# Performance work log

Measured on AMD Instinct MI355X. Metric: run time of the kernel, lower is better.

## Reference

```python
import jax, jax.numpy as jnp
import numpy as np

B, S, HID = 2, 2048, 4096
NH, NKV = 32, 8
HD = HID // NH          # 128
G = NH // NKV           # 4 groups per kv head
ROPE_THETA = 10000.0


def setup_inputs() -> dict:
    key = jax.random.key(0)
    ks = jax.random.split(key, 5)
    scale = 0.02
    return {
        "hidden_states": jax.random.normal(ks[0], (B, S, HID), dtype=jnp.float32),
        "Wq": jax.random.normal(ks[1], (NH * HD, HID), dtype=jnp.float32) * scale,
        "Wk": jax.random.normal(ks[2], (NKV * HD, HID), dtype=jnp.float32) * scale,
        "Wv": jax.random.normal(ks[3], (NKV * HD, HID), dtype=jnp.float32) * scale,
        "Wo": jax.random.normal(ks[4], (HID, HID), dtype=jnp.float32) * scale,
    }


def _rope_cos_sin(seq_len, head_dim, dtype):
    inv_freq = 1.0 / (ROPE_THETA ** (jnp.arange(0, head_dim, 2, dtype=jnp.float32) / head_dim))
    pos = jnp.arange(seq_len, dtype=jnp.float32)
    freqs = pos[:, None] * inv_freq[None, :]          # [S, HD/2]
    emb = jnp.concatenate([freqs, freqs], axis=-1)    # [S, HD]  (Llama: duplicated halves)
    return jnp.cos(emb).astype(dtype), jnp.sin(emb).astype(dtype)


def _rotate_half(x):
    x1, x2 = jnp.split(x, 2, axis=-1)
    return jnp.concatenate([-x2, x1], axis=-1)


def _apply_rope(x, cos, sin):
    # x: [B, H, S, HD]; cos/sin: [S, HD]
    return x * cos[None, None] + _rotate_half(x) * sin[None, None]


def reference(hidden_states, Wq, Wk, Wv, Wo):
    bsz, q_len, _ = hidden_states.shape
    dt = hidden_states.dtype

    q = (hidden_states @ Wq.T).reshape(bsz, q_len, NH, HD).transpose(0, 2, 1, 3)    # [B,NH,S,HD]
    k = (hidden_states @ Wk.T).reshape(bsz, q_len, NKV, HD).transpose(0, 2, 1, 3)   # [B,NKV,S,HD]
    v = (hidden_states @ Wv.T).reshape(bsz, q_len, NKV, HD).transpose(0, 2, 1, 3)   # [B,NKV,S,HD]

    cos, sin = _rope_cos_sin(q_len, HD, dt)
    q = _apply_rope(q, cos, sin)
    k = _apply_rope(k, cos, sin)

    # GQA: group queries per kv head instead of materializing repeat_kv
    qg = q.reshape(bsz, NKV, G, q_len, HD)                                          # [B,NKV,G,S,HD]
    scores = jnp.einsum("bkgqd,bkvd->bkgqv", qg, k) * (1.0 / np.sqrt(HD))           # [B,NKV,G,S,S]

    causal = jnp.tril(jnp.ones((q_len, q_len), dtype=bool))
    scores = jnp.where(causal[None, None, None], scores, jnp.finfo(jnp.float32).min)

    probs = jax.nn.softmax(scores.astype(jnp.float32), axis=-1).astype(dt)
    out = jnp.einsum("bkgqv,bkvd->bkgqd", probs, v)                                 # [B,NKV,G,S,HD]
    out = out.reshape(bsz, NH, q_len, HD).transpose(0, 2, 1, 3).reshape(bsz, q_len, HID)
    return out @ Wo.T
```

## Files before the change

### kernel.cpp

```cpp
#include <hip/hip_runtime.h>

typedef unsigned short u16;
typedef unsigned int u32;
typedef __attribute__((ext_vector_type(8))) short short8;
typedef __attribute__((ext_vector_type(4))) float f32x4;
typedef __attribute__((ext_vector_type(4))) u16 ushort4_t;

__device__ __forceinline__ float bf2f(u16 u) {
    u32 x = ((u32)u) << 16;
    return __uint_as_float(x);
}
__device__ __forceinline__ u16 f2bf(float f) {
    u32 x = __float_as_uint(f);
    x += 0x7FFFu + ((x >> 16) & 1u);
    return (u16)(x >> 16);
}
__device__ __forceinline__ u32 cvtpk_bf16(float lo, float hi) {
    u32 r;
    asm("v_cvt_pk_bf16_f32 %0, %1, %2" : "=v"(r) : "v"(lo), "v"(hi));
    return r;
}
__device__ __forceinline__ float exp2_hw(float x) {
    float r;
    asm("v_exp_f32 %0, %1" : "=v"(r) : "v"(x));
    return r;
}

using as1_cv = __attribute__((address_space(1))) const void;
using as3_v  = __attribute__((address_space(3))) void;
__device__ __forceinline__ void gld16(const void* g, void* l) {
    __builtin_amdgcn_global_load_lds((as1_cv*)g, (as3_v*)l, 16, 0, 0);
}

__global__ void cvt_f32_bf16(const float* __restrict__ in, u16* __restrict__ out, int n4) {
    int i = blockIdx.x * 256 + threadIdx.x;
    if (i >= n4) return;
    float4 v = ((const float4*)in)[i];
    ushort4_t o;
    o[0] = f2bf(v.x); o[1] = f2bf(v.y); o[2] = f2bf(v.z); o[3] = f2bf(v.w);
    ((ushort4_t*)out)[i] = o;
}

template <int OUT_MODE>
__global__ __launch_bounds__(256) void gemm_bt(
    const u16* __restrict__ A, const u16* __restrict__ B,
    u16* __restrict__ Cb, float* __restrict__ Cf,
    int M, int N, int K)
{
    __shared__ __align__(16) u16 As[128 * 32];
    __shared__ __align__(16) u16 Bs[128 * 32];
    const int t    = threadIdx.x;
    const int lane = t & 63;
    const int w    = t >> 6;
    const int wm   = w & 1;
    const int wn   = w >> 1;
    const int bx   = blockIdx.x;
    const int by   = blockIdx.y;

    const int r  = t >> 2;
    const int c8 = (t & 3) * 8;
    const u16* gA0 = A + (size_t)(by * 128 + r) * K + c8;
    const u16* gA1 = gA0 + (size_t)64 * K;
    const u16* gB0 = B + (size_t)(bx * 128 + r) * K + c8;
    const u16* gB1 = gB0 + (size_t)64 * K;
    u16* lA0 = &As[t * 8];
    u16* lA1 = &As[2048 + t * 8];
    u16* lB0 = &Bs[t * 8];
    u16* lB1 = &Bs[2048 + t * 8];

    f32x4 acc[4][4] = {};

    const int arow = wm * 64 + (lane & 15);
    const int brow = wn * 64 + (lane & 15);
    const int koff = (lane >> 4) * 8;

    for (int kt = 0; kt < K; kt += 32) {
        gld16(gA0 + kt, lA0);
        gld16(gA1 + kt, lA1);
        gld16(gB0 + kt, lB0);
        gld16(gB1 + kt, lB1);
        __syncthreads();
        short8 af[4], bf[4];
#pragma unroll
        for (int i = 0; i < 4; i++)
            af[i] = *(const short8*)&As[(arow + i * 16) * 32 + koff];
#pragma unroll
        for (int i = 0; i < 4; i++)
            bf[i] = *(const short8*)&Bs[(brow + i * 16) * 32 + koff];
#pragma unroll
        for (int mi = 0; mi < 4; mi++)
#pragma unroll
            for (int ni = 0; ni < 4; ni++)
                acc[mi][ni] = __builtin_amdgcn_mfma_f32_16x16x32_bf16(
                    af[mi], bf[ni], acc[mi][ni], 0, 0, 0);
        __syncthreads();
    }

    const int row0 = by * 128 + wm * 64 + (lane >> 4) * 4;
    const int col0 = bx * 128 + wn * 64 + (lane & 15);
#pragma unroll
    for (int mi = 0; mi < 4; mi++) {
#pragma unroll
        for (int ni = 0; ni < 4; ni++) {
            if (OUT_MODE == 3) {
                ushort4_t o;
#pragma unroll
                for (int rr = 0; rr < 4; rr++) o[rr] = f2bf(acc[mi][ni][rr]);
                int col = col0 + ni * 16;
                *(ushort4_t*)&Cb[(size_t)col * M + row0 + mi * 16] = o;
            } else {
#pragma unroll
                for (int rr = 0; rr < 4; rr++) {
                    int row = row0 + mi * 16 + rr;
                    int col = col0 + ni * 16;
                    float v = acc[mi][ni][rr];
                    if (OUT_MODE == 1) Cf[(size_t)row * N + col] = v;
                    else               Cb[(size_t)row * N + col] = f2bf(v);
                }
            }
        }
    }
}

template <int OUT_MODE>
__global__ __launch_bounds__(512, 2) void gemm_bt256(
    const u16* __restrict__ A, const u16* __restrict__ B,
    u16* __restrict__ Cb, float* __restrict__ Cf,
    int M, int N, int K)
{
    __shared__ __align__(16) u16 S[65536];
    const int t    = threadIdx.x;
    const int lane = t & 63;
    const int w    = t >> 6;
    const int wm   = w >> 2;
    const int wn   = w & 3;
    const int col  = lane & 15;
    const int g    = lane >> 4;

    const int kel = (((t & 3) ^ ((t >> 4) & 3)) * 8);
    const u16* gA = A + (size_t)(blockIdx.y * 256 + (t >> 2)) * K + kel;
    const u16* gB = B + (size_t)(blockIdx.x * 256 + (t >> 2)) * K + kel;
    const size_t rstride = (size_t)128 * K;
    u16* ldsA = &S[t * 8];
    u16* ldsB = &S[8192 + t * 8];

    const int rchunk = (((col * 4 + g) ^ ((col >> 2) & 3)) * 8);
    int aoff[8], boff[4];
#pragma unroll
    for (int mi = 0; mi < 8; mi++) aoff[mi] = (wm * 8 + mi) * 512 + rchunk;
#pragma unroll
    for (int ni = 0; ni < 4; ni++) boff[ni] = 8192 + (wn * 4 + ni) * 512 + rchunk;

    f32x4 acc[8][4] = {};

    auto STAGE = [&](int slot, int kt) {
        const size_t so = (size_t)slot * 16384;
        gld16(gA + kt,            ldsA + so);
        gld16(gA + kt + rstride,  ldsA + so + 4096);
        gld16(gB + kt,            ldsB + so);
        gld16(gB + kt + rstride,  ldsB + so + 4096);
    };

    const int NT = K >> 5;
    STAGE(0, 0);
    STAGE(1, 32);
    STAGE(2, 64);

    for (int kt = 0; kt < NT; kt++) {
        if (kt < NT - 2)      asm volatile("s_waitcnt vmcnt(8)" ::: "memory");
        else if (kt < NT - 1) asm volatile("s_waitcnt vmcnt(4)" ::: "memory");
        else                  asm volatile("s_waitcnt vmcnt(0)" ::: "memory");
        __builtin_amdgcn_s_barrier();
        asm volatile("" ::: "memory");
        if (kt < NT - 3) STAGE((kt + 3) & 3, (kt + 3) << 5);

        const u16* Sb = &S[(kt & 3) * 16384];
        short8 af[8], bf[4];
#pragma unroll
        for (int mi = 0; mi < 8; mi++) af[mi] = *(const short8*)(Sb + aoff[mi]);
#pragma unroll
        for (int ni = 0; ni < 4; ni++) bf[ni] = *(const short8*)(Sb + boff[ni]);

        __builtin_amdgcn_s_setprio(1);
#pragma unroll
        for (int mi = 0; mi < 8; mi++)
#pragma unroll
            for (int ni = 0; ni < 4; ni++)
                acc[mi][ni] = __builtin_amdgcn_mfma_f32_16x16x32_bf16(
                    af[mi], bf[ni], acc[mi][ni], 0, 0, 0);
        __builtin_amdgcn_s_setprio(0);
    }

    const int row0 = blockIdx.y * 256 + wm * 128 + (lane >> 4) * 4;
    const int col0 = blockIdx.x * 256 + wn * 64 + (lane & 15);
#pragma unroll
    for (int mi = 0; mi < 8; mi++) {
#pragma unroll
        for (int ni = 0; ni < 4; ni++) {
#pragma unroll
            for (int rr = 0; rr < 4; rr++) {
                int row = row0 + mi * 16 + rr;
                int col = col0 + ni * 16;
                float v = acc[mi][ni][rr];
                if (OUT_MODE == 1) Cf[(size_t)row * N + col] = v;
                else               Cb[(size_t)row * N + col] = f2bf(v);
            }
        }
    }
}

__global__ void rope_k(u16* __restrict__ x, int hshift, float scale) {
    int idx = blockIdx.x * 256 + threadIdx.x;
    int i   = idx & 63;
    int hm  = (1 << (hshift - 6)) - 1;
    int h   = (idx >> 6) & hm;
    int row = idx >> hshift;
    int s   = row & 2047;
    int stride = (hm + 1) * 128;
    size_t base = (size_t)row * stride + h * 128 + i;
    float th = (float)s * exp2f(-(float)i * 0.20762050593045952f);
    float cs = cosf(th), sn = sinf(th);
    float x1 = bf2f(x[base]), x2 = bf2f(x[base + 64]);
    x[base]      = f2bf((x1 * cs - x2 * sn) * scale);
    x[base + 64] = f2bf((x2 * cs + x1 * sn) * scale);
}

__global__ __launch_bounds__(512) void flash_attn(
    const u16* __restrict__ qb, const u16* __restrict__ kb,
    const u16* __restrict__ vt, u16* __restrict__ ob)
{
    __shared__ __align__(16) u16 Ks[3][64 * 128];
    __shared__ __align__(16) u16 Vs[3][128 * 64];
    const int t    = threadIdx.x;
    const int lane = t & 63;
    const int w    = t >> 6;
    const int col  = lane & 15;
    const int g    = lane >> 4;
    const int p    = blockIdx.x;
    const int qh   = blockIdx.y;
    const int b    = blockIdx.z;
    const int kvh  = qh >> 2;

    const u16* kbase = kb + ((size_t)b * 2048) * 1024 + kvh * 128;
    const u16* vbase = vt + ((size_t)kvh * 128) * 4096 + (size_t)b * 2048;

    const int ksw = ((t >> 4) & 3) ^ (((t >> 4) & 8) >> 1);
    const u16* ksrc0 = kbase + (size_t)(t >> 4) * 1024 + (size_t)((t & 15) ^ ksw) * 8;
    const u16* vsrc0 = vbase + (size_t)(t >> 3) * 4096 + (size_t)(((t & 7) ^ ((t >> 3) & 7)) * 8);
    u16* kdst = &Ks[0][0] + t * 8;
    u16* vdst = &Vs[0][0] + t * 8;

    const int swr = (col & 3) ^ (((col >> 2) & 1) << 2);
    int kb_[2][2];
#pragma unroll
    for (int h = 0; h < 2; h++)
#pragma unroll
        for (int kk = 0; kk < 2; kk++)
            kb_[h][kk] = (h * 32 + (col >> 2) * 8 + kk * 4 + (col & 3)) * 16;
    int cco[4];
#pragma unroll
    for (int c = 0; c < 4; c++) cco[c] = (c * 4 + g) ^ swr;
    const int vrow = col * 8;
    const int vcc0 = (g) ^ (col & 7);
    const int vcc1 = (4 + g) ^ (col & 7);

    auto STAGE = [&](int slot, int k0i) {
        const size_t so = (size_t)slot * 8192;
        gld16(ksrc0 + (size_t)k0i * 1024,        kdst + so);
        gld16(ksrc0 + (size_t)(k0i + 32) * 1024, kdst + so + 4096);
        gld16(vsrc0 + k0i,                       vdst + so);
        gld16(vsrc0 + (size_t)64 * 4096 + k0i,   vdst + so + 4096);
    };

#pragma unroll 1
    for (int phase = 0; phase < 2; phase++) {
        const int qt = phase ? (3 - p) : (4 + p);
        const int Q0 = qt * 256;
        const int qw = Q0 + w * 32;

        short8 qf[2][4];
#pragma unroll
        for (int sub = 0; sub < 2; sub++) {
            const u16* qrow = qb + ((size_t)(b * 2048 + qw + sub * 16 + col)) * 4096 + qh * 128;
#pragma unroll
            for (int c = 0; c < 4; c++)
                qf[sub][c] = *(const short8*)(qrow + c * 32 + g * 8);
        }

        float m_run[2] = {0.f, 0.f};
        float l_run[2] = {0.f, 0.f};
        f32x4 ot[2][8] = {};

        const int nsteps = (Q0 + 256) >> 6;
        const int qmax_w = qw + 31;

        STAGE(0, 0);
        STAGE(1, 64);
        int slc = 0;

        for (int step = 0; step < nsteps; step++) {
            const int k0 = step << 6;
            if (step + 1 < nsteps) asm volatile("s_waitcnt vmcnt(4)" ::: "memory");
            else                   asm volatile("s_waitcnt vmcnt(0)" ::: "memory");
            __builtin_amdgcn_s_barrier();
            asm volatile("" ::: "memory");
            if (step + 2 < nsteps) {
                int sl2 = slc + 2; if (sl2 >= 3) sl2 -= 3;
                STAGE(sl2, (step + 2) << 6);
            }

            if (k0 <= qmax_w) {
                const u16* Kp = &Ks[slc][0];
                const u16* Vp = &Vs[slc][0];

                f32x4 sc[2][2][2] = {};
                __builtin_amdgcn_s_setprio(1);
#pragma unroll
                for (int h = 0; h < 2; h++)
#pragma unroll
                    for (int c = 0; c < 4; c++)
#pragma unroll
                        for (int kk = 0; kk < 2; kk++) {
                            short8 kf = *(const short8*)(Kp + (size_t)(kb_[h][kk] + cco[c]) * 8);
                            sc[0][h][kk] = __builtin_amdgcn_mfma_f32_16x16x32_bf16(kf, qf[0][c], sc[0][h][kk], 0, 0, 0);
                            sc[1][h][kk] = __builtin_amdgcn_mfma_f32_16x16x32_bf16(kf, qf[1][c], sc[1][h][kk], 0, 0, 0);
                        }
                __builtin_amdgcn_s_setprio(0);

                const bool full = (k0 + 63 <= qw);
                short8 pf[2][2];
#pragma unroll
                for (int sub = 0; sub < 2; sub++) {
                    float s[16];
                    float tmax = -1e30f;
                    if (full) {
#pragma unroll
                        for (int h = 0; h < 2; h++)
#pragma unroll
                            for (int kk = 0; kk < 2; kk++)
#pragma unroll
                                for (int rr = 0; rr < 4; rr++) {
                                    float v = sc[sub][h][kk][rr];
                                    s[h * 8 + kk * 4 + rr] = v;
                                    tmax = fmaxf(tmax, v);
                                }
                    } else {
                        const int q = qw + sub * 16 + col;
#pragma unroll
                        for (int h = 0; h < 2; h++)
#pragma unroll
                            for (int kk = 0; kk < 2; kk++)
#pragma unroll
                                for (int rr = 0; rr < 4; rr++) {
                                    int key = k0 + h * 32 + g * 8 + kk * 4 + rr;
                                    float v = sc[sub][h][kk][rr];
                                    v = (key <= q) ? v : -1e30f;
                                    s[h * 8 + kk * 4 + rr] = v;
                                    tmax = fmaxf(tmax, v);
                                }
                    }
                    tmax = fmaxf(tmax, __shfl_xor(tmax, 16));
                    tmax = fmaxf(tmax, __shfl_xor(tmax, 32));
                    if (__any(tmax > m_run[sub] + 8.0f)) {
                        float m_new = fmaxf(m_run[sub], tmax);
                        float alpha = exp2_hw(m_run[sub] - m_new);
                        l_run[sub] *= alpha;
                        m_run[sub] = m_new;
#pragma unroll
                        for (int dt = 0; dt < 8; dt++)
#pragma unroll
                            for (int rr = 0; rr < 4; rr++) ot[sub][dt][rr] *= alpha;
                    }
                    const float m = m_run[sub];
                    float tsum = 0.f;
#pragma unroll
                    for (int j = 0; j < 16; j++) {
                        s[j] = exp2_hw(s[j] - m);
                        tsum += s[j];
                    }
#pragma unroll
                    for (int h = 0; h < 2; h++)
#pragma unroll
                        for (int jw = 0; jw < 4; jw++)
                            ((u32*)&pf[sub][h])[jw] = cvtpk_bf16(s[h * 8 + jw * 2], s[h * 8 + jw * 2 + 1]);
                    tsum += __shfl_xor(tsum, 16);
                    tsum += __shfl_xor(tsum, 32);
                    l_run[sub] += tsum;
                }

                __builtin_amdgcn_s_setprio(1);
#pragma unroll
                for (int dt = 0; dt < 8; dt++) {
                    short8 vf0 = *(const short8*)(Vp + (size_t)(dt * 128 + vrow + vcc0) * 8);
                    short8 vf1 = *(const short8*)(Vp + (size_t)(dt * 128 + vrow + vcc1) * 8);
                    ot[0][dt] = __builtin_amdgcn_mfma_f32_16x16x32_bf16(vf0, pf[0][0], ot[0][dt], 0, 0, 0);
                    ot[1][dt] = __builtin_amdgcn_mfma_f32_16x16x32_bf16(vf0, pf[1][0], ot[1][dt], 0, 0, 0);
                    ot[0][dt] = __builtin_amdgcn_mfma_f32_16x16x32_bf16(vf1, pf[0][1], ot[0][dt], 0, 0, 0);
                    ot[1][dt] = __builtin_amdgcn_mfma_f32_16x16x32_bf16(vf1, pf[1][1], ot[1][dt], 0, 0, 0);
                }
                __builtin_amdgcn_s_setprio(0);
            }
            slc = (slc == 2) ? 0 : slc + 1;
        }
        __syncthreads();

#pragma unroll
        for (int sub = 0; sub < 2; sub++) {
            float inv = 1.0f / l_run[sub];
            u16* orow = ob + ((size_t)(b * 2048 + qw + sub * 16 + col)) * 4096 + qh * 128;
#pragma unroll
            for (int dt = 0; dt < 8; dt++) {
                ushort4_t o;
#pragma unroll
                for (int rr = 0; rr < 4; rr++) o[rr] = f2bf(ot[sub][dt][rr] * inv);
                *(ushort4_t*)(orow + dt * 16 + g * 4) = o;
            }
        }
    }
}

extern "C" void kernel_launch(void* const* d_in, const int* in_sizes, int n_in,
                              void* d_out, int out_size, void* d_ws, size_t ws_size,
                              hipStream_t stream) {
    const float* hs = (const float*)d_in[0];
    const float* Wq = (const float*)d_in[1];
    const float* Wk = (const float*)d_in[2];
    const float* Wv = (const float*)d_in[3];
    const float* Wo = (const float*)d_in[4];
    float* out = (float*)d_out;

    char* ws = (char*)d_ws;
    u16* hsb = (u16*)(ws + 0);
    u16* Wqb = (u16*)(ws + 33554432);
    u16* Wkb = (u16*)(ws + 67108864);
    u16* Wvb = (u16*)(ws + 75497472);
    u16* Wob = (u16*)(ws + 83886080);
    u16* qb  = (u16*)(ws + 117440512);
    u16* kbf = (u16*)(ws + 150994944);
    u16* vtb = (u16*)(ws + 159383552);
    u16* ab  = hsb;

    cvt_f32_bf16<<<16384, 256, 0, stream>>>(hs, hsb, 4194304);
    cvt_f32_bf16<<<16384, 256, 0, stream>>>(Wq, Wqb, 4194304);
    cvt_f32_bf16<<<4096,  256, 0, stream>>>(Wk, Wkb, 1048576);
    cvt_f32_bf16<<<4096,  256, 0, stream>>>(Wv, Wvb, 1048576);
    cvt_f32_bf16<<<16384, 256, 0, stream>>>(Wo, Wob, 4194304);

    gemm_bt256<0><<<dim3(16, 16), 512, 0, stream>>>(hsb, Wqb, qb,  nullptr, 4096, 4096, 4096);
    gemm_bt<0><<<dim3(8, 32),  256, 0, stream>>>(hsb, Wkb, kbf, nullptr, 4096, 1024, 4096);
    gemm_bt<3><<<dim3(8, 32),  256, 0, stream>>>(hsb, Wvb, vtb, nullptr, 4096, 1024, 4096);

    rope_k<<<32768, 256, 0, stream>>>(qb,  11, 0.08838834764831845f * 1.4426950408889634f);
    rope_k<<<8192,  256, 0, stream>>>(kbf, 9, 1.0f);

    flash_attn<<<dim3(4, 32, 2), 512, 0, stream>>>(qb, kbf, vtb, ab);

    gemm_bt256<1><<<dim3(16, 16), 512, 0, stream>>>(ab, Wob, nullptr, out, 4096, 4096, 4096);
}
```

Measured before the change: 782.4 us.

## Restructure GEMM main loop into 8-phase ping-pong schedule with interleaved loads

The 256x256 GEMM K-loop moves from a 4-slot ring of 32-wide K tiles to two 64-wide K buffers. Each iteration is split into four phases, and each phase interleaves LDS fragment reads, one half-tile global prefetch, barriers and a block of MFMAs. The aim is finer overlap of global loads, LDS reads and matrix math, with reads pinned in place by sched_barrier and setprio. The cost is many more block barriers per iteration and fragile hand-tuned vmcnt accounting that must match the issue order.

Result: no change. 796.0 us (+1.7%).

```diff
diff --git a/kernel.cpp b/kernel.cpp
--- a/kernel.cpp
+++ b/kernel.cpp
@@ -141,54 +141,107 @@
     const u16* gA = A + (size_t)(blockIdx.y * 256 + (t >> 2)) * K + kel;
     const u16* gB = B + (size_t)(blockIdx.x * 256 + (t >> 2)) * K + kel;
     const size_t rstride = (size_t)128 * K;
-    u16* ldsA = &S[t * 8];
-    u16* ldsB = &S[8192 + t * 8];
 
     const int rchunk = (((col * 4 + g) ^ ((col >> 2) & 3)) * 8);
     int aoff[8], boff[4];
 #pragma unroll
     for (int mi = 0; mi < 8; mi++) aoff[mi] = (wm * 8 + mi) * 512 + rchunk;
 #pragma unroll
-    for (int ni = 0; ni < 4; ni++) boff[ni] = 8192 + (wn * 4 + ni) * 512 + rchunk;
+    for (int ni = 0; ni < 4; ni++) boff[ni] = (wn * 4 + ni) * 512 + rchunk;
 
     f32x4 acc[8][4] = {};
 
-    auto STAGE = [&](int slot, int kt) {
-        const size_t so = (size_t)slot * 16384;
-        gld16(gA + kt,            ldsA + so);
-        gld16(gA + kt + rstride,  ldsA + so + 4096);
-        gld16(gB + kt,            ldsB + so);
-        gld16(gB + kt + rstride,  ldsB + so + 4096);
+    auto STAGE_H = [&](int b, int op, int kh, int kt) {
+        const u16* gsrc = op ? gB : gA;
+        u16* dst = &S[b * 32768 + kh * 16384 + op * 8192 + t * 8];
+        const int ko = (kt << 6) + (kh << 5);
+        gld16(gsrc + ko, dst);
+        gld16(gsrc + ko + rstride, dst + 4096);
     };
 
-    const int NT = K >> 5;
-    STAGE(0, 0);
-    STAGE(1, 32);
-    STAGE(2, 64);
+    const int NT = K >> 6;
+
+    STAGE_H(0, 0, 0, 0); STAGE_H(0, 1, 0, 0); STAGE_H(0, 0, 1, 0); STAGE_H(0, 1, 1, 0);
+    STAGE_H(1, 0, 0, 1); STAGE_H(1, 1, 0, 1); STAGE_H(1, 0, 1, 1);
+    asm volatile("s_waitcnt vmcnt(6)" ::: "memory");
+    __builtin_amdgcn_s_barrier();
 
     for (int kt = 0; kt < NT; kt++) {
-        if (kt < NT - 2)      asm volatile("s_waitcnt vmcnt(8)" ::: "memory");
-        else if (kt < NT - 1) asm volatile("s_waitcnt vmcnt(4)" ::: "memory");
-        else                  asm volatile("s_waitcnt vmcnt(0)" ::: "memory");
-        __builtin_amdgcn_s_barrier();
-        asm volatile("" ::: "memory");
-        if (kt < NT - 3) STAGE((kt + 3) & 3, (kt + 3) << 5);
-
-        const u16* Sb = &S[(kt & 3) * 16384];
-        short8 af[8], bf[4];
-#pragma unroll
-        for (int mi = 0; mi < 8; mi++) af[mi] = *(const short8*)(Sb + aoff[mi]);
-#pragma unroll
-        for (int ni = 0; ni < 4; ni++) bf[ni] = *(const short8*)(Sb + boff[ni]);
-
+        const int b = kt & 1;
+        const u16* Ak0 = &S[b * 32768];
+        const u16* Bk0 = &S[b * 32768 + 8192];
+        const u16* Ak1 = &S[b * 32768 + 16384];
+        const u16* Bk1 = &S[b * 32768 + 24576];
+
+        short8 af0[8], bf00, bf01;
+#pragma unroll
+        for (int mi = 0; mi < 8; mi++) af0[mi] = *(const short8*)(Ak0 + aoff[mi]);
+        bf00 = *(const short8*)(Bk0 + boff[0]);
+        bf01 = *(const short8*)(Bk0 + boff[1]);
+        if (kt + 1 < NT) STAGE_H(b ^ 1, 1, 1, kt + 1);
+        __builtin_amdgcn_s_barrier();
+        asm volatile("s_waitcnt lgkmcnt(0)" ::: "memory");
+        __builtin_amdgcn_sched_barrier(0);
         __builtin_amdgcn_s_setprio(1);
 #pragma unroll
-        for (int mi = 0; mi < 8; mi++)
-#pragma unroll
-            for (int ni = 0; ni < 4; ni++)
-                acc[mi][ni] = __builtin_amdgcn_mfma_f32_16x16x32_bf16(
-                    af[mi], bf[ni], acc[mi][ni], 0, 0, 0);
+        for (int mi = 0; mi < 8; mi++) {
+            acc[mi][0] = __builtin_amdgcn_mfma_f32_16x16x32_bf16(af0[mi], bf00, acc[mi][0], 0, 0, 0);
+            acc[mi][1] = __builtin_amdgcn_mfma_f32_16x16x32_bf16(af0[mi], bf01, acc[mi][1], 0, 0, 0);
+        }
         __builtin_amdgcn_s_setprio(0);
+        __builtin_amdgcn_s_barrier();
+
+        short8 bf02, bf03;
+        bf02 = *(const short8*)(Bk0 + boff[2]);
+        bf03 = *(const short8*)(Bk0 + boff[3]);
+        if (kt + 2 < NT) STAGE_H(b, 0, 0, kt + 2);
+        __builtin_amdgcn_s_barrier();
+        asm volatile("s_waitcnt lgkmcnt(0)" ::: "memory");
+        __builtin_amdgcn_sched_barrier(0);
+        __builtin_amdgcn_s_setprio(1);
+#pragma unroll
+        for (int mi = 0; mi < 8; mi++) {
+            acc[mi][2] = __builtin_amdgcn_mfma_f32_16x16x32_bf16(af0[mi], bf02, acc[mi][2], 0, 0, 0);
+            acc[mi][3] = __builtin_amdgcn_mfma_f32_16x16x32_bf16(af0[mi], bf03, acc[mi][3], 0, 0, 0);
+        }
+        __builtin_amdgcn_s_setprio(0);
+        __builtin_amdgcn_s_barrier();
+
+        short8 af1[8], bf10, bf11;
+#pragma unroll
+        for (int mi = 0; mi < 8; mi++) af1[mi] = *(const short8*)(Ak1 + aoff[mi]);
+        bf10 = *(const short8*)(Bk1 + boff[0]);
+        bf11 = *(const short8*)(Bk1 + boff[1]);
+        if (kt + 2 < NT) STAGE_H(b, 1, 0, kt + 2);
+        __builtin_amdgcn_s_barrier();
+        asm volatile("s_waitcnt lgkmcnt(0)" ::: "memory");
+        __builtin_amdgcn_sched_barrier(0);
+        __builtin_amdgcn_s_setprio(1);
+#pragma unroll
+        for (int mi = 0; mi < 8; mi++) {
+            acc[mi][0] = __builtin_amdgcn_mfma_f32_16x16x32_bf16(af1[mi], bf10, acc[mi][0], 0, 0, 0);
+            acc[mi][1] = __builtin_amdgcn_mfma_f32_16x16x32_bf16(af1[mi], bf11, acc[mi][1], 0, 0, 0);
+        }
+        __builtin_amdgcn_s_setprio(0);
+        __builtin_amdgcn_s_barrier();
+
+        short8 bf12, bf13;
+        bf12 = *(const short8*)(Bk1 + boff[2]);
+        bf13 = *(const short8*)(Bk1 + boff[3]);
+        if (kt + 2 < NT) STAGE_H(b, 0, 1, kt + 2);
+        __builtin_amdgcn_s_barrier();
+        asm volatile("s_waitcnt lgkmcnt(0)" ::: "memory");
+        __builtin_amdgcn_sched_barrier(0);
+        __builtin_amdgcn_s_setprio(1);
+#pragma unroll
+        for (int mi = 0; mi < 8; mi++) {
+            acc[mi][2] = __builtin_amdgcn_mfma_f32_16x16x32_bf16(af1[mi], bf12, acc[mi][2], 0, 0, 0);
+            acc[mi][3] = __builtin_amdgcn_mfma_f32_16x16x32_bf16(af1[mi], bf13, acc[mi][3], 0, 0, 0);
+        }
+        __builtin_amdgcn_s_setprio(0);
+        if (kt + 2 < NT)      asm volatile("s_waitcnt vmcnt(6)" ::: "memory");
+        else if (kt + 1 < NT) asm volatile("s_waitcnt vmcnt(0)" ::: "memory");
+        __builtin_amdgcn_s_barrier();
     }
 
     const int row0 = blockIdx.y * 256 + wm * 128 + (lane >> 4) * 4;
```
